# Optimization experiments

Measured on AMD Instinct MI355X. Metric: run time of the kernel, lower is better.

## Reference

```python
import jax, jax.numpy as jnp
import numpy as np

N_NODES = 50000
N_EDGES = 400000
N_GRAPHS = 512
IN_DIM = 768
HID = 64
BN_EPS = 1e-5


def setup_inputs() -> dict:
    key = jax.random.key(0)
    ks = jax.random.split(key, 12)
    x = jax.random.normal(ks[0], (N_NODES, IN_DIM), dtype=jnp.float32)
    edge_index = jax.random.randint(ks[1], (2, N_EDGES), 0, N_NODES, dtype=jnp.int64)
    batch = jnp.sort(jax.random.randint(ks[2], (N_NODES,), 0, N_GRAPHS, dtype=jnp.int64))

    def lin_init(k, fan_in, fan_out):
        kw, kb = jax.random.split(k)
        bound = 1.0 / np.sqrt(fan_in)
        W = jax.random.uniform(kw, (fan_in, fan_out), minval=-bound, maxval=bound, dtype=jnp.float32)
        b = jax.random.uniform(kb, (fan_out,), minval=-bound, maxval=bound, dtype=jnp.float32)
        return W, b

    w1a, b1a = lin_init(ks[3], IN_DIM, HID)
    w1b, b1b = lin_init(ks[4], HID, HID)
    w2a, b2a = lin_init(ks[5], HID, HID)
    w2b, b2b = lin_init(ks[6], HID, HID)
    wl, bl = lin_init(ks[7], 2 * HID, 2)

    ones = jnp.ones((HID,), jnp.float32)
    zeros = jnp.zeros((HID,), jnp.float32)
    return {
        "x": x, "edge_index": edge_index, "batch": batch,
        "w1a": w1a, "b1a": b1a, "g1": ones, "be1": zeros, "rm1": zeros, "rv1": ones,
        "w1b": w1b, "b1b": b1b,
        "w2a": w2a, "b2a": b2a, "g2": ones, "be2": zeros, "rm2": zeros, "rv2": ones,
        "w2b": w2b, "b2b": b2b,
        "wl": wl, "bl": bl,
    }


def _bn_eval(h, gamma, beta, rm, rv):
    # BatchNorm1d in eval mode: normalize with running stats
    return (h - rm) * (gamma * jax.lax.rsqrt(rv + BN_EPS)) + beta


def _gin_conv(x, src, dst, Wa, ba, gamma, beta, rm, rv, Wb, bb):
    # GINConv eps=0: h = MLP(x + sum_{j in N(i)} x_j); messages x[src] scatter-added to dst
    agg = jax.ops.segment_sum(x[src], dst, num_segments=N_NODES)
    h = x + agg
    h = jnp.dot(h, Wa) + ba
    h = jax.nn.relu(_bn_eval(h, gamma, beta, rm, rv))
    return jnp.dot(h, Wb) + bb


def reference(x, edge_index, batch,
              w1a, b1a, g1, be1, rm1, rv1, w1b, b1b,
              w2a, b2a, g2, be2, rm2, rv2, w2b, b2b,
              wl, bl):
    src, dst = edge_index[0], edge_index[1]
    # eval mode: dropout_edge and F.dropout are identity
    x1 = jax.nn.relu(_gin_conv(x, src, dst, w1a, b1a, g1, be1, rm1, rv1, w1b, b1b))
    x2 = jax.nn.relu(_gin_conv(x1, src, dst, w2a, b2a, g2, be2, rm2, rv2, w2b, b2b))
    x_jk = jnp.concatenate([x1, x2], axis=-1)  # [N, 2*HID]
    x_pool = jax.ops.segment_sum(x_jk, batch, num_segments=N_GRAPHS)  # [G, 2*HID]
    return jnp.dot(x_pool, wl) + bl  # [G, 2]
```

## Files before the change

### kernel.cpp

```cpp
#include <hip/hip_runtime.h>

constexpr int N_NODES  = 50000;
constexpr int N_EDGES  = 400000;
constexpr int N_GRAPHS = 512;
constexpr int IN_DIM   = 768;
constexpr int HID      = 64;
constexpr float BN_EPS = 1e-5f;
constexpr int CAP      = 64;

typedef __attribute__((ext_vector_type(8))) short bf16x8;
typedef __attribute__((ext_vector_type(4))) float f32x4;

__device__ __forceinline__ float bf2f(ushort u) {
  return __uint_as_float((unsigned int)u << 16);
}
__device__ __forceinline__ ushort f2bf(float f) {
  unsigned int u = __float_as_uint(f);
  u = (u + 0x7fff + ((u >> 16) & 1)) >> 16;
  return (ushort)u;
}

constexpr int W1A_E = HID * IN_DIM;
constexpr int WB_E  = HID * HID;
__global__ __launch_bounds__(256) void convert_all(
    const float* __restrict__ w1a, const float* __restrict__ w1b,
    const float* __restrict__ w2a, const float* __restrict__ w2b,
    const float* __restrict__ bl,
    ushort* __restrict__ WT, ushort* __restrict__ WT1b,
    ushort* __restrict__ WT2a, ushort* __restrict__ WT2b,
    float* __restrict__ out) {
  int i = blockIdx.x * 256 + threadIdx.x;
  if (i < W1A_E) {
    int c = i / IN_DIM, k = i - c * IN_DIM;
    WT[i] = f2bf(w1a[(size_t)k * HID + c]);
    return;
  }
  int j = i - W1A_E;
  if (j < 3 * WB_E) {
    int w = j / WB_E, r = j - w * WB_E;
    int c = r / HID, k = r - c * HID;
    const float* W = (w == 0) ? w1b : (w == 1) ? w2a : w2b;
    ushort* D = (w == 0) ? WT1b : (w == 1) ? WT2a : WT2b;
    D[r] = f2bf(W[(size_t)k * HID + c]);
    return;
  }
  int o = j - 3 * WB_E;
  if (o < N_GRAPHS * 2) out[o] = bl[o & 1];
}

__global__ __launch_bounds__(256) void gemm_in_mfma(const float* __restrict__ X,
                                                    const ushort* __restrict__ WT,
                                                    ushort* __restrict__ P) {
  __shared__ ushort xs[64][64];
  __shared__ ushort ws[64][64];
  const int tid  = threadIdx.x;
  const int row0 = blockIdx.x * 64;
  const int wave = tid >> 6;
  const int lane = tid & 63;
  const int quad = lane >> 4;
  const int l16  = lane & 15;

  const int srow = tid >> 2;
  const int sk   = (tid & 3) * 16;
  const int ch0  = ((sk >> 3) + 0) ^ (srow & 7);
  const int ch1  = ((sk >> 3) + 1) ^ (srow & 7);

  int gr = row0 + srow;
  gr = gr < N_NODES ? gr : N_NODES - 1;
  const float*  xrow = &X[(size_t)gr * IN_DIM + sk];
  const ushort* wrow = &WT[(size_t)srow * IN_DIM + sk];

  f32x4 acc[4] = {};

  float4 xv0 = *(const float4*)&xrow[0];
  float4 xv1 = *(const float4*)&xrow[4];
  float4 xv2 = *(const float4*)&xrow[8];
  float4 xv3 = *(const float4*)&xrow[12];
  uint4  wv0 = *(const uint4*)&wrow[0];
  uint4  wv1 = *(const uint4*)&wrow[8];

  for (int kt = 0; kt < IN_DIM; kt += 64) {
    ushort xb[16];
    {
      float xv[16] = {xv0.x, xv0.y, xv0.z, xv0.w, xv1.x, xv1.y, xv1.z, xv1.w,
                      xv2.x, xv2.y, xv2.z, xv2.w, xv3.x, xv3.y, xv3.z, xv3.w};
#pragma unroll
      for (int i = 0; i < 16; i++) xb[i] = f2bf(xv[i]);
    }
    *(uint4*)&xs[srow][ch0 * 8] = *(uint4*)&xb[0];
    *(uint4*)&xs[srow][ch1 * 8] = *(uint4*)&xb[8];
    *(uint4*)&ws[srow][ch0 * 8] = wv0;
    *(uint4*)&ws[srow][ch1 * 8] = wv1;
    __syncthreads();

    if (kt + 64 < IN_DIM) {
      xv0 = *(const float4*)&xrow[kt + 64 + 0];
      xv1 = *(const float4*)&xrow[kt + 64 + 4];
      xv2 = *(const float4*)&xrow[kt + 64 + 8];
      xv3 = *(const float4*)&xrow[kt + 64 + 12];
      wv0 = *(const uint4*)&wrow[kt + 64 + 0];
      wv1 = *(const uint4*)&wrow[kt + 64 + 8];
    }

    const int ar   = wave * 16 + l16;
    const int axor = ar & 7;
#pragma unroll
    for (int ks = 0; ks < 2; ks++) {
      bf16x8 a = *(const bf16x8*)&xs[ar][((ks * 4 + quad) ^ axor) * 8];
#pragma unroll
      for (int ct = 0; ct < 4; ct++) {
        const int br = ct * 16 + l16;
        bf16x8 b = *(const bf16x8*)&ws[br][((ks * 4 + quad) ^ (br & 7)) * 8];
        acc[ct] = __builtin_amdgcn_mfma_f32_16x16x32_bf16(a, b, acc[ct], 0, 0, 0);
      }
    }
    __syncthreads();
  }

#pragma unroll
  for (int ct = 0; ct < 4; ct++) {
#pragma unroll
    for (int r = 0; r < 4; r++) {
      int row = row0 + wave * 16 + quad * 4 + r;
      if (row < N_NODES) P[(size_t)row * HID + ct * 16 + l16] = f2bf(acc[ct][r]);
    }
  }
}

__global__ __launch_bounds__(256) void build_buckets(const int* __restrict__ src,
                                                     const int* __restrict__ dst,
                                                     int* __restrict__ cnt,
                                                     int* __restrict__ bucket) {
  int e = blockIdx.x * 256 + threadIdx.x;
  if (e >= N_EDGES) return;
  int s = src[e];
  int d = dst[e];
  int slot = atomicAdd(&cnt[d], 1);
  if (slot < CAP) bucket[d * CAP + slot] = s;
}

__global__ __launch_bounds__(256) void gather_agg(const int* __restrict__ cnt,
                                                  const int* __restrict__ bucket,
                                                  const ushort* __restrict__ P,
                                                  ushort* __restrict__ AGG) {
  int n = blockIdx.x * 4 + (threadIdx.x >> 6);
  n = __builtin_amdgcn_readfirstlane(n);
  int lane = threadIdx.x & 63;
  if (n >= N_NODES) return;
  int c = cnt[n];
  c = c < CAP ? c : CAP;
  const int* b = &bucket[n * CAP];
  float acc = 0.0f;
  int i = 0;
  for (; i + 4 <= c; i += 4) {
    int s0 = b[i + 0], s1 = b[i + 1], s2 = b[i + 2], s3 = b[i + 3];
    float v0 = bf2f(P[(size_t)s0 * HID + lane]);
    float v1 = bf2f(P[(size_t)s1 * HID + lane]);
    float v2 = bf2f(P[(size_t)s2 * HID + lane]);
    float v3 = bf2f(P[(size_t)s3 * HID + lane]);
    acc += (v0 + v1) + (v2 + v3);
  }
  for (; i < c; i++) acc += bf2f(P[(size_t)b[i] * HID + lane]);
  AGG[(size_t)n * HID + lane] = f2bf(acc);
}

__global__ __launch_bounds__(256) void mlp64_mfma(
    const ushort* __restrict__ A, const ushort* __restrict__ AGG,
    const float* __restrict__ bin, const float* __restrict__ g,
    const float* __restrict__ be, const float* __restrict__ rm,
    const float* __restrict__ rv, const ushort* __restrict__ WT,
    const float* __restrict__ bout, ushort* __restrict__ OUT,
    int has_bn, int relu_out) {
  __shared__ ushort xs[64][64];
  __shared__ ushort ws[64][64];
  __shared__ float sS[64], sT[64];
  const int tid  = threadIdx.x;
  const int row0 = blockIdx.x * 64;
  const int srow = tid >> 2;
  const int qc0  = (tid & 3) * 2;

  if (tid < 64 && has_bn) {
    float s = g[tid] * rsqrtf(rv[tid] + BN_EPS);
    sS[tid] = s;
    sT[tid] = (bin[tid] - rm[tid]) * s + be[tid];
  }
  {
    uint4 w0 = *(const uint4*)&WT[(size_t)srow * HID + qc0 * 8];
    uint4 w1 = *(const uint4*)&WT[(size_t)srow * HID + qc0 * 8 + 8];
    *(uint4*)&ws[srow][((qc0 + 0) ^ (srow & 7)) * 8] = w0;
    *(uint4*)&ws[srow][((qc0 + 1) ^ (srow & 7)) * 8] = w1;
  }
  __syncthreads();

  {
    int gr = row0 + srow;
    gr = gr < N_NODES ? gr : N_NODES - 1;
    ushort va[16];
    *(uint4*)&va[0] = *(const uint4*)&A[(size_t)gr * HID + qc0 * 8];
    *(uint4*)&va[8] = *(const uint4*)&A[(size_t)gr * HID + qc0 * 8 + 8];
    if (has_bn) {
      ushort vg[16];
      *(uint4*)&vg[0] = *(const uint4*)&AGG[(size_t)gr * HID + qc0 * 8];
      *(uint4*)&vg[8] = *(const uint4*)&AGG[(size_t)gr * HID + qc0 * 8 + 8];
#pragma unroll
      for (int j = 0; j < 16; j++) {
        int col = qc0 * 8 + j;
        float v = bf2f(va[j]) + bf2f(vg[j]);
        v = fmaxf(fmaf(v, sS[col], sT[col]), 0.0f);
        va[j] = f2bf(v);
      }
    }
    *(uint4*)&xs[srow][((qc0 + 0) ^ (srow & 7)) * 8] = *(uint4*)&va[0];
    *(uint4*)&xs[srow][((qc0 + 1) ^ (srow & 7)) * 8] = *(uint4*)&va[8];
  }
  __syncthreads();

  const int wave = tid >> 6, lane = tid & 63, quad = lane >> 4, l16 = lane & 15;
  f32x4 acc[4] = {};
  const int ar   = wave * 16 + l16;
  const int axor = ar & 7;
#pragma unroll
  for (int ks = 0; ks < 2; ks++) {
    bf16x8 a = *(const bf16x8*)&xs[ar][((ks * 4 + quad) ^ axor) * 8];
#pragma unroll
    for (int ct = 0; ct < 4; ct++) {
      const int br = ct * 16 + l16;
      bf16x8 b = *(const bf16x8*)&ws[br][((ks * 4 + quad) ^ (br & 7)) * 8];
      acc[ct] = __builtin_amdgcn_mfma_f32_16x16x32_bf16(a, b, acc[ct], 0, 0, 0);
    }
  }

#pragma unroll
  for (int ct = 0; ct < 4; ct++) {
    const int col = ct * 16 + l16;
    float bo = bout ? bout[col] : 0.0f;
#pragma unroll
    for (int r = 0; r < 4; r++) {
      int row = row0 + wave * 16 + quad * 4 + r;
      if (row < N_NODES) {
        float v = acc[ct][r] + bo;
        if (relu_out) v = fmaxf(v, 0.0f);
        OUT[(size_t)row * HID + col] = f2bf(v);
      }
    }
  }
}

__global__ __launch_bounds__(256) void pool2(const ushort* __restrict__ x1,
                                             const ushort* __restrict__ x2,
                                             const int* __restrict__ batch,
                                             const float* __restrict__ wl,
                                             float* __restrict__ out) {
  __shared__ float gacc[N_GRAPHS * 2];
  __shared__ float wl_s[2 * HID * 2];
  const int tid = threadIdx.x;
#pragma unroll
  for (int i = tid; i < N_GRAPHS * 2; i += 256) gacc[i] = 0.0f;
  wl_s[tid] = wl[tid];
  __syncthreads();

  const int wave = tid >> 6, lane = tid & 63;
  const int sub = lane & 3, noff = lane >> 2;
  const int nbase = blockIdx.x * 256 + wave * 64;
#pragma unroll
  for (int it = 0; it < 4; it++) {
    int node = nbase + it * 16 + noff;
    bool ok = node < N_NODES;
    int cn = ok ? node : N_NODES - 1;
    ushort v1[16], v2[16];
    const ushort* r1 = &x1[(size_t)cn * HID + sub * 16];
    const ushort* r2 = &x2[(size_t)cn * HID + sub * 16];
    *(uint4*)&v1[0] = *(const uint4*)&r1[0];
    *(uint4*)&v1[8] = *(const uint4*)&r1[8];
    *(uint4*)&v2[0] = *(const uint4*)&r2[0];
    *(uint4*)&v2[8] = *(const uint4*)&r2[8];
    float p0 = 0.0f, p1 = 0.0f;
#pragma unroll
    for (int j = 0; j < 16; j++) {
      int e = sub * 16 + j;
      float a = bf2f(v1[j]);
      float b = bf2f(v2[j]);
      p0 += a * wl_s[e * 2 + 0] + b * wl_s[(HID + e) * 2 + 0];
      p1 += a * wl_s[e * 2 + 1] + b * wl_s[(HID + e) * 2 + 1];
    }
    p0 += __shfl_xor(p0, 1); p0 += __shfl_xor(p0, 2);
    p1 += __shfl_xor(p1, 1); p1 += __shfl_xor(p1, 2);
    if (sub == 0 && ok) {
      int gr = batch[node];
      atomicAdd(&gacc[gr * 2 + 0], p0);
      atomicAdd(&gacc[gr * 2 + 1], p1);
    }
  }
  __syncthreads();
#pragma unroll
  for (int i = tid; i < N_GRAPHS * 2; i += 256) {
    float v = gacc[i];
    if (v != 0.0f) atomicAdd(&out[i], v);
  }
}

extern "C" void kernel_launch(void* const* d_in, const int* in_sizes, int n_in,
                              void* d_out, int out_size, void* d_ws, size_t ws_size,
                              hipStream_t stream) {
  const float* x   = (const float*)d_in[0];
  const int*   ei  = (const int*)d_in[1];
  const int*   bat = (const int*)d_in[2];
  const float* w1a = (const float*)d_in[3];
  const float* b1a = (const float*)d_in[4];
  const float* g1  = (const float*)d_in[5];
  const float* be1 = (const float*)d_in[6];
  const float* rm1 = (const float*)d_in[7];
  const float* rv1 = (const float*)d_in[8];
  const float* w1b = (const float*)d_in[9];
  const float* b1b = (const float*)d_in[10];
  const float* w2a = (const float*)d_in[11];
  const float* b2a = (const float*)d_in[12];
  const float* g2  = (const float*)d_in[13];
  const float* be2 = (const float*)d_in[14];
  const float* rm2 = (const float*)d_in[15];
  const float* rv2 = (const float*)d_in[16];
  const float* w2b = (const float*)d_in[17];
  const float* b2b = (const float*)d_in[18];
  const float* wl  = (const float*)d_in[19];
  const float* bl  = (const float*)d_in[20];
  float* out = (float*)d_out;

  const int* src = ei;
  const int* dst = ei + N_EDGES;

  const size_t FB = (size_t)N_NODES * HID;
  ushort* P    = (ushort*)d_ws;
  ushort* AGG  = P + FB;
  ushort* X1   = AGG + FB;
  ushort* X2   = X1 + FB;
  ushort* WT   = X2 + FB;
  ushort* WT1b = WT + (size_t)W1A_E;
  ushort* WT2a = WT1b + WB_E;
  ushort* WT2b = WT2a + WB_E;
  int* cnt     = (int*)(WT2b + WB_E);
  int* bucket  = cnt + N_NODES;

  const int GB = (N_NODES + 63) / 64;
  const int BB = (N_EDGES + 255) / 256;
  const int AB = N_NODES / 4;
  const int PB = (N_NODES + 255) / 256;
  const int CB = (W1A_E + 3 * WB_E + N_GRAPHS * 2 + 255) / 256;

  hipMemsetAsync(cnt, 0, N_NODES * sizeof(int), stream);
  build_buckets<<<BB, 256, 0, stream>>>(src, dst, cnt, bucket);
  convert_all<<<CB, 256, 0, stream>>>(w1a, w1b, w2a, w2b, bl,
                                      WT, WT1b, WT2a, WT2b, out);

  gemm_in_mfma<<<GB, 256, 0, stream>>>(x, WT, P);
  gather_agg<<<AB, 256, 0, stream>>>(cnt, bucket, P, AGG);
  mlp64_mfma<<<GB, 256, 0, stream>>>(P, AGG, b1a, g1, be1, rm1, rv1, WT1b, b1b,
                                     X1, 1, 1);
  mlp64_mfma<<<GB, 256, 0, stream>>>(X1, nullptr, nullptr, nullptr, nullptr,
                                     nullptr, nullptr, WT2a, nullptr, P, 0, 0);
  gather_agg<<<AB, 256, 0, stream>>>(cnt, bucket, P, AGG);
  mlp64_mfma<<<GB, 256, 0, stream>>>(P, AGG, b2a, g2, be2, rm2, rv2, WT2b, b2b,
                                     X2, 1, 1);
  pool2<<<PB, 256, 0, stream>>>(X1, X2, bat, wl, out);
}
```

Before: 362.9 us.

## Fuse neighbor gather into MLP kernels and chain second layer's first GEMM

The separate gather_agg kernel is folded into the MLP kernel: each block gathers neighbor rows for its 64 nodes with 16-wide vector loads (4 threads per node), adds the self row, applies BN+ReLU and runs the MFMA GEMM. Layer 1's output GEMM is chained in the same kernel with the next layer's input projection, so the AGG buffer and two launches go away. The cnt memset moves into convert_all. In exchange, the gather now runs with less parallelism per node (4 threads per node instead of a wave), which may hurt latency hiding on the random loads.

```diff
diff --git a/kernel.cpp b/kernel.cpp
--- a/kernel.cpp
+++ b/kernel.cpp
@@ -28,7 +28,7 @@
     const float* __restrict__ bl,
     ushort* __restrict__ WT, ushort* __restrict__ WT1b,
     ushort* __restrict__ WT2a, ushort* __restrict__ WT2b,
-    float* __restrict__ out) {
+    float* __restrict__ out, int* __restrict__ cnt) {
   int i = blockIdx.x * 256 + threadIdx.x;
   if (i < W1A_E) {
     int c = i / IN_DIM, k = i - c * IN_DIM;
@@ -45,7 +45,9 @@
     return;
   }
   int o = j - 3 * WB_E;
-  if (o < N_GRAPHS * 2) out[o] = bl[o & 1];
+  if (o < N_GRAPHS * 2) { out[o] = bl[o & 1]; return; }
+  int z = o - N_GRAPHS * 2;
+  if (z < N_NODES) cnt[z] = 0;
 }
 
 __global__ __launch_bounds__(256) void gemm_in_mfma(const float* __restrict__ X,
@@ -139,86 +141,99 @@
   if (slot < CAP) bucket[d * CAP + slot] = s;
 }
 
-__global__ __launch_bounds__(256) void gather_agg(const int* __restrict__ cnt,
-                                                  const int* __restrict__ bucket,
-                                                  const ushort* __restrict__ P,
-                                                  ushort* __restrict__ AGG) {
-  int n = blockIdx.x * 4 + (threadIdx.x >> 6);
-  n = __builtin_amdgcn_readfirstlane(n);
-  int lane = threadIdx.x & 63;
-  if (n >= N_NODES) return;
-  int c = cnt[n];
-  c = c < CAP ? c : CAP;
-  const int* b = &bucket[n * CAP];
-  float acc = 0.0f;
-  int i = 0;
-  for (; i + 4 <= c; i += 4) {
-    int s0 = b[i + 0], s1 = b[i + 1], s2 = b[i + 2], s3 = b[i + 3];
-    float v0 = bf2f(P[(size_t)s0 * HID + lane]);
-    float v1 = bf2f(P[(size_t)s1 * HID + lane]);
-    float v2 = bf2f(P[(size_t)s2 * HID + lane]);
-    float v3 = bf2f(P[(size_t)s3 * HID + lane]);
-    acc += (v0 + v1) + (v2 + v3);
-  }
-  for (; i < c; i++) acc += bf2f(P[(size_t)b[i] * HID + lane]);
-  AGG[(size_t)n * HID + lane] = f2bf(acc);
-}
-
-__global__ __launch_bounds__(256) void mlp64_mfma(
-    const ushort* __restrict__ A, const ushort* __restrict__ AGG,
+template <int CHAIN>
+__global__ __launch_bounds__(256) void fused_mlp(
+    const int* __restrict__ cnt, const int* __restrict__ bucket,
+    const ushort* __restrict__ Pin,
     const float* __restrict__ bin, const float* __restrict__ g,
     const float* __restrict__ be, const float* __restrict__ rm,
-    const float* __restrict__ rv, const ushort* __restrict__ WT,
-    const float* __restrict__ bout, ushort* __restrict__ OUT,
-    int has_bn, int relu_out) {
+    const float* __restrict__ rv,
+    const ushort* __restrict__ WT1, const float* __restrict__ b1,
+    const ushort* __restrict__ WT2,
+    ushort* __restrict__ OUT1, ushort* __restrict__ OUT2) {
   __shared__ ushort xs[64][64];
   __shared__ ushort ws[64][64];
+  __shared__ ushort ws2[64][64];
   __shared__ float sS[64], sT[64];
   const int tid  = threadIdx.x;
   const int row0 = blockIdx.x * 64;
   const int srow = tid >> 2;
-  const int qc0  = (tid & 3) * 2;
-
-  if (tid < 64 && has_bn) {
+  const int sub  = tid & 3;
+  const int qc0  = sub * 2;
+
+  if (tid < 64) {
     float s = g[tid] * rsqrtf(rv[tid] + BN_EPS);
     sS[tid] = s;
     sT[tid] = (bin[tid] - rm[tid]) * s + be[tid];
   }
   {
-    uint4 w0 = *(const uint4*)&WT[(size_t)srow * HID + qc0 * 8];
-    uint4 w1 = *(const uint4*)&WT[(size_t)srow * HID + qc0 * 8 + 8];
+    uint4 w0 = *(const uint4*)&WT1[(size_t)srow * HID + qc0 * 8];
+    uint4 w1 = *(const uint4*)&WT1[(size_t)srow * HID + qc0 * 8 + 8];
     *(uint4*)&ws[srow][((qc0 + 0) ^ (srow & 7)) * 8] = w0;
     *(uint4*)&ws[srow][((qc0 + 1) ^ (srow & 7)) * 8] = w1;
+    if (CHAIN) {
+      uint4 v0 = *(const uint4*)&WT2[(size_t)srow * HID + qc0 * 8];
+      uint4 v1 = *(const uint4*)&WT2[(size_t)srow * HID + qc0 * 8 + 8];
+      *(uint4*)&ws2[srow][((qc0 + 0) ^ (srow & 7)) * 8] = v0;
+      *(uint4*)&ws2[srow][((qc0 + 1) ^ (srow & 7)) * 8] = v1;
+    }
   }
   __syncthreads();
 
   {
-    int gr = row0 + srow;
-    gr = gr < N_NODES ? gr : N_NODES - 1;
-    ushort va[16];
-    *(uint4*)&va[0] = *(const uint4*)&A[(size_t)gr * HID + qc0 * 8];
-    *(uint4*)&va[8] = *(const uint4*)&A[(size_t)gr * HID + qc0 * 8 + 8];
-    if (has_bn) {
-      ushort vg[16];
-      *(uint4*)&vg[0] = *(const uint4*)&AGG[(size_t)gr * HID + qc0 * 8];
-      *(uint4*)&vg[8] = *(const uint4*)&AGG[(size_t)gr * HID + qc0 * 8 + 8];
-#pragma unroll
-      for (int j = 0; j < 16; j++) {
-        int col = qc0 * 8 + j;
-        float v = bf2f(va[j]) + bf2f(vg[j]);
-        v = fmaxf(fmaf(v, sS[col], sT[col]), 0.0f);
-        va[j] = f2bf(v);
-      }
-    }
-    *(uint4*)&xs[srow][((qc0 + 0) ^ (srow & 7)) * 8] = *(uint4*)&va[0];
-    *(uint4*)&xs[srow][((qc0 + 1) ^ (srow & 7)) * 8] = *(uint4*)&va[8];
+    int node = row0 + srow;
+    node = node < N_NODES ? node : N_NODES - 1;
+    float acc[16];
+    {
+      ushort b0[16];
+      const ushort* base = &Pin[(size_t)node * HID + sub * 16];
+      *(uint4*)&b0[0] = *(const uint4*)&base[0];
+      *(uint4*)&b0[8] = *(const uint4*)&base[8];
+#pragma unroll
+      for (int j = 0; j < 16; j++) acc[j] = bf2f(b0[j]);
+    }
+    int c = cnt[node];
+    c = c < CAP ? c : CAP;
+    const int* bkt = &bucket[node * CAP];
+    int i = 0;
+    for (; i + 4 <= c; i += 4) {
+      int4 s4 = *(const int4*)&bkt[i];
+      ushort r0[16], r1[16], r2[16], r3[16];
+      const ushort* p0 = &Pin[(size_t)s4.x * HID + sub * 16];
+      const ushort* p1 = &Pin[(size_t)s4.y * HID + sub * 16];
+      const ushort* p2 = &Pin[(size_t)s4.z * HID + sub * 16];
+      const ushort* p3 = &Pin[(size_t)s4.w * HID + sub * 16];
+      *(uint4*)&r0[0] = *(const uint4*)&p0[0]; *(uint4*)&r0[8] = *(const uint4*)&p0[8];
+      *(uint4*)&r1[0] = *(const uint4*)&p1[0]; *(uint4*)&r1[8] = *(const uint4*)&p1[8];
+      *(uint4*)&r2[0] = *(const uint4*)&p2[0]; *(uint4*)&r2[8] = *(const uint4*)&p2[8];
+      *(uint4*)&r3[0] = *(const uint4*)&p3[0]; *(uint4*)&r3[8] = *(const uint4*)&p3[8];
+#pragma unroll
+      for (int j = 0; j < 16; j++)
+        acc[j] += (bf2f(r0[j]) + bf2f(r1[j])) + (bf2f(r2[j]) + bf2f(r3[j]));
+    }
+    for (; i < c; i++) {
+      const ushort* p0 = &Pin[(size_t)bkt[i] * HID + sub * 16];
+      ushort r0[16];
+      *(uint4*)&r0[0] = *(const uint4*)&p0[0]; *(uint4*)&r0[8] = *(const uint4*)&p0[8];
+#pragma unroll
+      for (int j = 0; j < 16; j++) acc[j] += bf2f(r0[j]);
+    }
+    ushort hb[16];
+#pragma unroll
+    for (int j = 0; j < 16; j++) {
+      int col = sub * 16 + j;
+      float v = fmaxf(fmaf(acc[j], sS[col], sT[col]), 0.0f);
+      hb[j] = f2bf(v);
+    }
+    *(uint4*)&xs[srow][((qc0 + 0) ^ (srow & 7)) * 8] = *(uint4*)&hb[0];
+    *(uint4*)&xs[srow][((qc0 + 1) ^ (srow & 7)) * 8] = *(uint4*)&hb[8];
   }
   __syncthreads();
 
   const int wave = tid >> 6, lane = tid & 63, quad = lane >> 4, l16 = lane & 15;
-  f32x4 acc[4] = {};
-  const int ar   = wave * 16 + l16;
-  const int axor = ar & 7;
+  const int ar = wave * 16 + l16, axor = ar & 7;
+
+  f32x4 acc1[4] = {};
 #pragma unroll
   for (int ks = 0; ks < 2; ks++) {
     bf16x8 a = *(const bf16x8*)&xs[ar][((ks * 4 + quad) ^ axor) * 8];
@@ -226,21 +241,58 @@
     for (int ct = 0; ct < 4; ct++) {
       const int br = ct * 16 + l16;
       bf16x8 b = *(const bf16x8*)&ws[br][((ks * 4 + quad) ^ (br & 7)) * 8];
-      acc[ct] = __builtin_amdgcn_mfma_f32_16x16x32_bf16(a, b, acc[ct], 0, 0, 0);
-    }
-  }
-
+      acc1[ct] = __builtin_amdgcn_mfma_f32_16x16x32_bf16(a, b, acc1[ct], 0, 0, 0);
+    }
+  }
+
+  if (CHAIN) __syncthreads();
+
+  ushort hv[4][4];
 #pragma unroll
   for (int ct = 0; ct < 4; ct++) {
     const int col = ct * 16 + l16;
-    float bo = bout ? bout[col] : 0.0f;
+    const float bo = b1[col];
 #pragma unroll
     for (int r = 0; r < 4; r++) {
-      int row = row0 + wave * 16 + quad * 4 + r;
-      if (row < N_NODES) {
-        float v = acc[ct][r] + bo;
-        if (relu_out) v = fmaxf(v, 0.0f);
-        OUT[(size_t)row * HID + col] = f2bf(v);
+      int lrow = wave * 16 + quad * 4 + r;
+      int grow = row0 + lrow;
+      float v = fmaxf(acc1[ct][r] + bo, 0.0f);
+      ushort h = f2bf(v);
+      hv[ct][r] = h;
+      if (grow < N_NODES) OUT1[(size_t)grow * HID + col] = h;
+    }
+  }
+
+  if (CHAIN) {
+#pragma unroll
+    for (int ct = 0; ct < 4; ct++) {
+      const int col = ct * 16 + l16;
+#pragma unroll
+      for (int r = 0; r < 4; r++) {
+        int lrow = wave * 16 + quad * 4 + r;
+        xs[lrow][(((col >> 3) ^ (lrow & 7)) * 8) + (col & 7)] = hv[ct][r];
+      }
+    }
+    __syncthreads();
+
+    f32x4 acc2[4] = {};
+#pragma unroll
+    for (int ks = 0; ks < 2; ks++) {
+      bf16x8 a = *(const bf16x8*)&xs[ar][((ks * 4 + quad) ^ axor) * 8];
+#pragma unroll
+      for (int ct = 0; ct < 4; ct++) {
+        const int br = ct * 16 + l16;
+        bf16x8 b = *(const bf16x8*)&ws2[br][((ks * 4 + quad) ^ (br & 7)) * 8];
+        acc2[ct] = __builtin_amdgcn_mfma_f32_16x16x32_bf16(a, b, acc2[ct], 0, 0, 0);
+      }
+    }
+#pragma unroll
+    for (int ct = 0; ct < 4; ct++) {
+      const int col = ct * 16 + l16;
+#pragma unroll
+      for (int r = 0; r < 4; r++) {
+        int grow = row0 + wave * 16 + quad * 4 + r;
+        if (grow < N_NODES) OUT2[(size_t)grow * HID + col] = f2bf(acc2[ct][r]);
       }
     }
   }
@@ -329,9 +381,9 @@
   const int* dst = ei + N_EDGES;
 
   const size_t FB = (size_t)N_NODES * HID;
-  ushort* P    = (ushort*)d_ws;
-  ushort* AGG  = P + FB;
-  ushort* X1   = AGG + FB;
+  ushort* P1   = (ushort*)d_ws;
+  ushort* P2   = P1 + FB;
+  ushort* X1   = P2 + FB;
   ushort* X2   = X1 + FB;
   ushort* WT   = X2 + FB;
   ushort* WT1b = WT + (size_t)W1A_E;
@@ -342,23 +394,17 @@
 
   const int GB = (N_NODES + 63) / 64;
   const int BB = (N_EDGES + 255) / 256;
-  const int AB = N_NODES / 4;
   const int PB = (N_NODES + 255) / 256;
-  const int CB = (W1A_E + 3 * WB_E + N_GRAPHS * 2 + 255) / 256;
-
-  hipMemsetAsync(cnt, 0, N_NODES * sizeof(int), stream);
+  const int CB = (W1A_E + 3 * WB_E + N_GRAPHS * 2 + N_NODES + 255) / 256;
+
+  convert_all<<<CB, 256, 0, stream>>>(w1a, w1b, w2a, w2b, bl,
+                                      WT, WT1b, WT2a, WT2b, out, cnt);
   build_buckets<<<BB, 256, 0, stream>>>(src, dst, cnt, bucket);
-  convert_all<<<CB, 256, 0, stream>>>(w1a, w1b, w2a, w2b, bl,
-                                      WT, WT1b, WT2a, WT2b, out);
-
-  gemm_in_mfma<<<GB, 256, 0, stream>>>(x, WT, P);
-  gather_agg<<<AB, 256, 0, stream>>>(cnt, bucket, P, AGG);
-  mlp64_mfma<<<GB, 256, 0, stream>>>(P, AGG, b1a, g1, be1, rm1, rv1, WT1b, b1b,
-                                     X1, 1, 1);
-  mlp64_mfma<<<GB, 256, 0, stream>>>(X1, nullptr, nullptr, nullptr, nullptr,
-                                     nullptr, nullptr, WT2a, nullptr, P, 0, 0);
-  gather_agg<<<AB, 256, 0, stream>>>(cnt, bucket, P, AGG);
-  mlp64_mfma<<<GB, 256, 0, stream>>>(P, AGG, b2a, g2, be2, rm2, rv2, WT2b, b2b,
-                                     X2, 1, 1);
+
+  gemm_in_mfma<<<GB, 256, 0, stream>>>(x, WT, P1);
+  fused_mlp<1><<<GB, 256, 0, stream>>>(cnt, bucket, P1, b1a, g1, be1, rm1, rv1,
+                                       WT1b, b1b, WT2a, X1, P2);
+  fused_mlp<0><<<GB, 256, 0, stream>>>(cnt, bucket, P2, b2a, g2, be2, rm2, rv2,
+                                       WT2b, b2b, nullptr, X2, nullptr);
   pool2<<<PB, 256, 0, stream>>>(X1, X2, bat, wl, out);
 }
```

Result: faster. 334.3 us (-7.9%).
